# Performance work log

Measured on AMD Instinct MI355X. Metric: run time of the kernel, lower is better.

Reference implementation:

```python
import jax, jax.numpy as jnp
import numpy as np

B, C, L = 16, 64, 512
L_P = 16
D_MODEL = 1024
STRIDE = 8
N_P = (L - L_P) // STRIDE + 2  # 64 patches
PERIOD = L // 2                # statsmodels period = series_input_length / 2


def setup_inputs() -> dict:
    key = jax.random.key(0)
    ks = jax.random.split(key, 11)
    s = 0.02  # small init scale for weights
    return {
        "data_x": jax.random.normal(ks[0], (B, C, L), jnp.float32),
        "gamma": jax.random.uniform(ks[1], (B, C, L), jnp.float32),
        "beta": jax.random.uniform(ks[2], (B, C, L), jnp.float32),
        "w_trend": jax.random.normal(ks[3], (L_P, L), jnp.float32) * s,
        "b_trend": jax.random.normal(ks[4], (L_P,), jnp.float32) * s,
        "w_seasonal": jax.random.normal(ks[5], (L_P, L), jnp.float32) * s,
        "b_seasonal": jax.random.normal(ks[6], (L_P,), jnp.float32) * s,
        "w_resid": jax.random.normal(ks[7], (L_P, L), jnp.float32) * s,
        "b_resid": jax.random.normal(ks[8], (L_P,), jnp.float32) * s,
        "w_g": jax.random.normal(ks[9], (D_MODEL, 3 * L_P), jnp.float32) * s,
        "b_g": jax.random.normal(ks[10], (D_MODEL,), jnp.float32) * s,
    }


def _decompose(x):
    """Vectorized statsmodels seasonal_decompose(model='additive', period=L//2).

    trend: centered moving average with filter [0.5,1,...,1,0.5]/p (even period),
           NaN edges -> replaced by 0 (as in the torch module).
    seasonal: per-phase nanmean of detrended, demeaned, tiled to length L.
    resid: detrended - seasonal on the valid (non-NaN) region, 0 elsewhere.
    x: [B, C, L] -> (trend, seasonal, resid) each [B, C, L].
    """
    p = PERIOD
    filt = jnp.concatenate([jnp.full((1,), 0.5, x.dtype),
                            jnp.ones((p - 1,), x.dtype),
                            jnp.full((1,), 0.5, x.dtype)]) / p  # len p+1 (p even)
    head = p // 2               # leading NaN count (filter is symmetric)
    nvalid = L - p              # valid trend samples
    xf = x.reshape(B * C, 1, L)
    tv = jax.lax.conv_general_dilated(xf, filt.reshape(1, 1, p + 1),
                                      (1,), "VALID")[:, 0, :]  # [BC, L-p]
    trend = jnp.zeros((B * C, L), x.dtype).at[:, head:head + nvalid].set(tv)
    dv = x.reshape(B * C, L)[:, head:head + nvalid] - tv  # detrended, valid region
    # per-phase nanmean over valid detrended samples
    phase = (head + jnp.arange(nvalid)) % p               # phase of each valid index
    sums = jnp.zeros((B * C, p), x.dtype).at[:, phase].add(dv)
    counts = jnp.zeros((p,), x.dtype).at[phase].add(1.0)
    pa = sums / counts                                    # period averages [BC, p]
    pa = pa - jnp.mean(pa, axis=1, keepdims=True)
    seasonal = jnp.tile(pa, (1, L // p))                  # L = 2p exactly
    resid = jnp.zeros((B * C, L), x.dtype).at[:, head:head + nvalid].set(
        dv - seasonal[:, head:head + nvalid])
    return (trend.reshape(B, C, L), seasonal.reshape(B, C, L),
            resid.reshape(B, C, L))


def reference(data_x, gamma, beta, w_trend, b_trend, w_seasonal, b_seasonal,
              w_resid, b_resid, w_g, b_g):
    # 'transformed': per-channel stats (dim=1), torch var is unbiased (ddof=1), epsi=0
    mean = jnp.mean(data_x, axis=1)
    var = jnp.var(data_x, axis=1, ddof=1)
    mean = (mean / jnp.sqrt(var))[:, None, :]             # [B,1,L] broadcast over C
    x = gamma * (data_x - mean) + beta
    x = jax.lax.stop_gradient(x)                          # season() detaches
    trend, seasonal, resid = _decompose(x)
    t = trend @ w_trend.T + b_trend                       # [B,C,L_p]
    s = seasonal @ w_seasonal.T + b_seasonal
    r = resid @ w_resid.T + b_resid
    feats = jnp.concatenate([t, s, r], axis=-1)           # [B,C,3*L_p]
    feats = jnp.broadcast_to(feats[:, :, None, :], (B, C, N_P, 3 * L_P))
    return feats @ w_g.T + b_g                            # [B,C,N_p,D_MODEL]
```

## Files before the change

### kernel.cpp

```cpp
#include <hip/hip_runtime.h>
#include <math.h>

#define BB   16
#define CC   64
#define LL   512
#define LP   16
#define DM   1024
#define NP   64
#define PRD  256
#define HEAD 128
#define NV   256

typedef float f32x4 __attribute__((ext_vector_type(4)));

#define OFF_MEANP 0
#define OFF_WSF   8192
#define OFF_WRS   (8192 + 4096)
#define OFF_FEATS 12304
#define OFF_RES   (12304 + 49152)

__global__ __launch_bounds__(256) void statsprep_kernel(
    const float* __restrict__ dx, const float* __restrict__ w_s,
    const float* __restrict__ w_r, float* __restrict__ ws)
{
    const int tid = threadIdx.x, bid = blockIdx.x;
    if (bid < 32) {
        int id = bid * 256 + tid;
        int b = id >> 9, l = id & 511;
        const float* p = dx + (size_t)b * CC * LL + l;
        float s = 0.f, sq = 0.f;
#pragma unroll 8
        for (int c = 0; c < CC; ++c) {
            float v = p[(size_t)c * LL];
            s += v; sq += v * v;
        }
        float mean = s * (1.0f / CC);
        float var  = (sq - (float)CC * mean * mean) * (1.0f / (CC - 1));
        ws[OFF_MEANP + id] = mean / sqrtf(var);
    } else {
#pragma unroll
        for (int idx = tid; idx < 16 * PRD; idx += 256) {
            int g = idx >> 8, m = idx & 255;
            ws[OFF_WSF + idx] = w_s[g * LL + m] + w_s[g * LL + PRD + m];
        }
        int g = tid >> 4, ln = tid & 15;
        float s = 0.f;
        for (int k = ln; k < PRD; k += 16) s += w_r[g * LL + HEAD + k];
#pragma unroll
        for (int m = 8; m; m >>= 1) s += __shfl_xor(s, m, 16);
        if (ln == 0) ws[OFF_WRS + g] = s;
    }
}

__global__ __launch_bounds__(256) void feats_kernel(
    const float* __restrict__ dx,    const float* __restrict__ gamma,
    const float* __restrict__ beta,  const float* __restrict__ w_t,
    const float* __restrict__ b_t,   const float* __restrict__ b_s,
    const float* __restrict__ b_r,   float* __restrict__ ws)
{
    __shared__ __align__(16) float xs[LL];
    __shared__ __align__(16) float pps[LL/2 + 1];
    __shared__ __align__(16) float tvs[NV];
    __shared__ __align__(16) float pas[PRD];
    __shared__ __align__(16) float feats[48];
    __shared__ float wsum[4];
    __shared__ float wred[4];

    const int tid  = threadIdx.x;
    const int lane = tid & 63;
    const int wv   = tid >> 6;
    const int bc   = blockIdx.x;
    const int b    = bc >> 6;

    const size_t base = (size_t)bc * LL;
    float2 xv = ((const float2*)(dx    + base))[tid];
    float2 gv = ((const float2*)(gamma + base))[tid];
    float2 bv = ((const float2*)(beta  + base))[tid];
    float2 mv = ((const float2*)(ws + OFF_MEANP + (size_t)b * LL))[tid];
    float2 xp;
    xp.x = gv.x * (xv.x - mv.x) + bv.x;
    xp.y = gv.y * (xv.y - mv.y) + bv.y;
    ((float2*)xs)[tid] = xp;

    float v = xp.x + xp.y;
#pragma unroll
    for (int d = 1; d < 64; d <<= 1) {
        float t = __shfl_up(v, d, 64);
        if (lane >= d) v += t;
    }
    if (lane == 63) wsum[wv] = v;
    __syncthreads();
    float off = 0.f;
    for (int w = 0; w < wv; ++w) off += wsum[w];
    pps[tid + 1] = v + off;
    if (tid == 0) pps[0] = 0.f;
    __syncthreads();

    const int i  = tid;
    const int k2 = i + 257;
    const float Pi = pps[i  >> 1] + ((i  & 1) ? xs[i  & ~1] : 0.f);
    const float Pk = pps[k2 >> 1] + ((k2 & 1) ? xs[k2 & ~1] : 0.f);
    const float tv = (Pk - Pi - 0.5f * (xs[i] + xs[i + 256])) * (1.0f / 256.0f);
    tvs[i] = tv;
    const float dv = xs[HEAD + i] - tv;

    float r = dv;
#pragma unroll
    for (int m = 32; m; m >>= 1) r += __shfl_xor(r, m, 64);
    if (lane == 0) wred[wv] = r;
    __syncthreads();
    const float mdv = (wred[0] + wred[1] + wred[2] + wred[3]) * (1.0f / 256.0f);

    pas[(i + 128) & 255] = dv - mdv;
    __syncthreads();

    {
        const int g  = tid >> 4;
        const int ln = tid & 15;
        const f32x4* wt4  = (const f32x4*)(w_t + g * LL + HEAD);
        const f32x4* wsf4 = (const f32x4*)(ws + OFF_WSF + g * PRD);
        const f32x4* tv4  = (const f32x4*)tvs;
        const f32x4* pa4  = (const f32x4*)pas;
        float at = 0.f, as = 0.f;
#pragma unroll
        for (int q = 0; q < 4; ++q) {
            const int m = ln * 4 + q;
            f32x4 t = tv4[m], p = pa4[m];
            f32x4 a = wt4[m], sfw = wsf4[m];
            at += t.x * a.x + t.y * a.y + t.z * a.z + t.w * a.w;
            as += p.x * sfw.x + p.y * sfw.y + p.z * sfw.z + p.w * sfw.w;
        }
#pragma unroll
        for (int msk = 8; msk; msk >>= 1) {
            at += __shfl_xor(at, msk, 64);
            as += __shfl_xor(as, msk, 64);
        }
        if (ln == 0) {
            feats[g]      = at + b_t[g];
            feats[16 + g] = as + b_s[g];
            feats[32 + g] = mdv * ws[OFF_WRS + g] + b_r[g];
        }
    }
    __syncthreads();

    if (tid < 12)
        ((f32x4*)(ws + OFF_FEATS))[bc * 12 + tid] = ((const f32x4*)feats)[tid];
}

__global__ __launch_bounds__(256) void gemm_kernel(
    const float* __restrict__ ws, const float* __restrict__ w_g,
    const float* __restrict__ b_g, float* __restrict__ resbuf)
{
    __shared__ f32x4 sfeat[64 * 12];
    const int tid    = threadIdx.x;
    const int bctile = blockIdx.x >> 4;
    const int dtile  = blockIdx.x & 15;

    const f32x4* fsrc = (const f32x4*)(ws + OFF_FEATS) + bctile * 64 * 12;
#pragma unroll
    for (int q = 0; q < 3; ++q) sfeat[q * 256 + tid] = fsrc[q * 256 + tid];
    __syncthreads();

    const int dl  = tid & 63, wid = tid >> 6;
    const int d   = dtile * 64 + dl;
    f32x4 wrow[12];
    const f32x4* wg4 = (const f32x4*)(w_g + (size_t)d * 48);
#pragma unroll
    for (int j = 0; j < 12; ++j) wrow[j] = wg4[j];
    const float bg = b_g[d];

    float* rb = resbuf + (size_t)(bctile * 64 + wid * 16) * DM + d;
#pragma unroll
    for (int r = 0; r < 16; ++r) {
        const f32x4* fr = &sfeat[(wid * 16 + r) * 12];
        float acc = bg;
#pragma unroll
        for (int j = 0; j < 12; ++j) {
            f32x4 f = fr[j], w = wrow[j];
            acc += f.x * w.x + f.y * w.y + f.z * w.z + f.w * w.w;
        }
        rb[(size_t)r * DM] = acc;
    }
}

__global__ __launch_bounds__(256) void bcast_kernel(
    const float* __restrict__ resbuf, float* __restrict__ out)
{
    const int tid = threadIdx.x;
    const int bc  = blockIdx.x >> 2;
    const int q   = blockIdx.x & 3;
    const f32x4 v = ((const f32x4*)resbuf)[bc * (DM / 4) + tid];
    f32x4* op = (f32x4*)out + (size_t)bc * (NP * DM / 4)
              + (size_t)q * 16 * (DM / 4) + tid;
#pragma unroll
    for (int n = 0; n < 16; ++n)
        op[(size_t)n * (DM / 4)] = v;
}

extern "C" void kernel_launch(void* const* d_in, const int* in_sizes, int n_in,
                              void* d_out, int out_size, void* d_ws, size_t ws_size,
                              hipStream_t stream) {
    const float* dx    = (const float*)d_in[0];
    const float* gamma = (const float*)d_in[1];
    const float* beta  = (const float*)d_in[2];
    const float* w_t   = (const float*)d_in[3];
    const float* b_t   = (const float*)d_in[4];
    const float* w_s   = (const float*)d_in[5];
    const float* b_s   = (const float*)d_in[6];
    const float* w_r   = (const float*)d_in[7];
    const float* b_r   = (const float*)d_in[8];
    const float* w_g   = (const float*)d_in[9];
    const float* b_g   = (const float*)d_in[10];
    float* out = (float*)d_out;
    float* ws  = (float*)d_ws;
    float* resbuf = ws + OFF_RES;

    statsprep_kernel<<<33, 256, 0, stream>>>(dx, w_s, w_r, ws);
    feats_kernel<<<BB * CC, 256, 0, stream>>>(
        dx, gamma, beta, w_t, b_t, b_s, b_r, ws);
    gemm_kernel<<<256, 256, 0, stream>>>(ws, w_g, b_g, resbuf);
    bcast_kernel<<<BB * CC * 4, 256, 0, stream>>>(resbuf, out);
}
```

Baseline: 74.93 us.

## Fuse feature, projection GEMM and broadcast into one per-row kernel

The feats, gemm and broadcast kernels are merged, so each block computes its 48 features, projects them through w_g for all 1024 outputs (four rows per thread), and writes the result directly to all 64 patch rows. This removes two launches and the workspace round trips for features and the GEMM result. In exchange every block rereads the full w_g matrix (192 KB, likely served from L2), and each block's output store grows to 256 KB, which reduces parallelism in the write phase. It also adds a launch_bounds occupancy hint.

```diff
diff --git a/kernel.cpp b/kernel.cpp
--- a/kernel.cpp
+++ b/kernel.cpp
@@ -16,8 +16,6 @@
 #define OFF_MEANP 0
 #define OFF_WSF   8192
 #define OFF_WRS   (8192 + 4096)
-#define OFF_FEATS 12304
-#define OFF_RES   (12304 + 49152)
 
 __global__ __launch_bounds__(256) void statsprep_kernel(
     const float* __restrict__ dx, const float* __restrict__ w_s,
@@ -52,11 +50,13 @@
     }
 }
 
-__global__ __launch_bounds__(256) void feats_kernel(
+__global__ __launch_bounds__(256, 4) void fused_kernel(
     const float* __restrict__ dx,    const float* __restrict__ gamma,
     const float* __restrict__ beta,  const float* __restrict__ w_t,
     const float* __restrict__ b_t,   const float* __restrict__ b_s,
-    const float* __restrict__ b_r,   float* __restrict__ ws)
+    const float* __restrict__ b_r,   const float* __restrict__ w_g,
+    const float* __restrict__ b_g,   const float* __restrict__ ws,
+    float* __restrict__ out)
 {
     __shared__ __align__(16) float xs[LL];
     __shared__ __align__(16) float pps[LL/2 + 1];
@@ -143,58 +143,33 @@
     }
     __syncthreads();
 
-    if (tid < 12)
-        ((f32x4*)(ws + OFF_FEATS))[bc * 12 + tid] = ((const f32x4*)feats)[tid];
-}
+    f32x4 f[12];
+    const f32x4* fr4 = (const f32x4*)feats;
+#pragma unroll
+    for (int j = 0; j < 12; ++j) f[j] = fr4[j];
 
-__global__ __launch_bounds__(256) void gemm_kernel(
-    const float* __restrict__ ws, const float* __restrict__ w_g,
-    const float* __restrict__ b_g, float* __restrict__ resbuf)
-{
-    __shared__ f32x4 sfeat[64 * 12];
-    const int tid    = threadIdx.x;
-    const int bctile = blockIdx.x >> 4;
-    const int dtile  = blockIdx.x & 15;
-
-    const f32x4* fsrc = (const f32x4*)(ws + OFF_FEATS) + bctile * 64 * 12;
+    const int d0 = tid * 4;
+    const f32x4 bg = ((const f32x4*)b_g)[tid];
+    float a[4];
 #pragma unroll
-    for (int q = 0; q < 3; ++q) sfeat[q * 256 + tid] = fsrc[q * 256 + tid];
-    __syncthreads();
-
-    const int dl  = tid & 63, wid = tid >> 6;
-    const int d   = dtile * 64 + dl;
-    f32x4 wrow[12];
-    const f32x4* wg4 = (const f32x4*)(w_g + (size_t)d * 48);
-#pragma unroll
-    for (int j = 0; j < 12; ++j) wrow[j] = wg4[j];
-    const float bg = b_g[d];
-
-    float* rb = resbuf + (size_t)(bctile * 64 + wid * 16) * DM + d;
-#pragma unroll
-    for (int r = 0; r < 16; ++r) {
-        const f32x4* fr = &sfeat[(wid * 16 + r) * 12];
-        float acc = bg;
+    for (int row = 0; row < 4; ++row) {
+        const f32x4* wg4 = (const f32x4*)(w_g + (size_t)(d0 + row) * 48);
+        float acc = 0.f;
 #pragma unroll
         for (int j = 0; j < 12; ++j) {
-            f32x4 f = fr[j], w = wrow[j];
-            acc += f.x * w.x + f.y * w.y + f.z * w.z + f.w * w.w;
+            f32x4 w = wg4[j];
+            acc += f[j].x * w.x + f[j].y * w.y + f[j].z * w.z + f[j].w * w.w;
         }
-        rb[(size_t)r * DM] = acc;
+        a[row] = acc;
     }
-}
+    f32x4 res;
+    res.x = a[0] + bg.x; res.y = a[1] + bg.y;
+    res.z = a[2] + bg.z; res.w = a[3] + bg.w;
 
-__global__ __launch_bounds__(256) void bcast_kernel(
-    const float* __restrict__ resbuf, float* __restrict__ out)
-{
-    const int tid = threadIdx.x;
-    const int bc  = blockIdx.x >> 2;
-    const int q   = blockIdx.x & 3;
-    const f32x4 v = ((const f32x4*)resbuf)[bc * (DM / 4) + tid];
-    f32x4* op = (f32x4*)out + (size_t)bc * (NP * DM / 4)
-              + (size_t)q * 16 * (DM / 4) + tid;
+    f32x4* op = (f32x4*)out + (size_t)bc * (NP * DM / 4) + tid;
 #pragma unroll
-    for (int n = 0; n < 16; ++n)
-        op[(size_t)n * (DM / 4)] = v;
+    for (int n = 0; n < NP; ++n)
+        op[(size_t)n * (DM / 4)] = res;
 }
 
 extern "C" void kernel_launch(void* const* d_in, const int* in_sizes, int n_in,
@@ -213,11 +188,8 @@
     const float* b_g   = (const float*)d_in[10];
     float* out = (float*)d_out;
     float* ws  = (float*)d_ws;
-    float* resbuf = ws + OFF_RES;
 
     statsprep_kernel<<<33, 256, 0, stream>>>(dx, w_s, w_r, ws);
-    feats_kernel<<<BB * CC, 256, 0, stream>>>(
-        dx, gamma, beta, w_t, b_t, b_s, b_r, ws);
-    gemm_kernel<<<256, 256, 0, stream>>>(ws, w_g, b_g, resbuf);
-    bcast_kernel<<<BB * CC * 4, 256, 0, stream>>>(resbuf, out);
+    fused_kernel<<<BB * CC, 256, 0, stream>>>(
+        dx, gamma, beta, w_t, b_t, b_s, b_r, w_g, b_g, ws, out);
 }
```

New measurement: 98.24 us. 31.1% more time.
